# Kernel tuning notes

Measured on AMD Instinct MI355X. Metric: run time of the kernel, lower is better.

The kernel has to match this reference:

```python
import jax, jax.numpy as jnp
import numpy as np

NUM_HEADS = 32
NUM_KV_HEADS = 8
HEAD_DIM = 128
SCALE = 0.08838834764831845  # head_dim ** -0.5
LENS = [1024, 900, 800, 700, 600, 500, 400, 300]  # ragged sequence lengths


def setup_inputs() -> dict:
    key = jax.random.key(0)
    kq, kk, kv = jax.random.split(key, 3)
    cu = np.concatenate([[0], np.cumsum(LENS)]).astype(np.int32)
    T = int(cu[-1])  # 5224 total tokens
    q = jax.random.normal(kq, (T, NUM_HEADS * HEAD_DIM), jnp.float32)
    k = jax.random.normal(kk, (T, NUM_KV_HEADS * HEAD_DIM), jnp.float32)
    v = jax.random.normal(kv, (T, NUM_KV_HEADS * HEAD_DIM), jnp.float32)
    return {"q": q, "k": k, "v": v, "cu_seqlens": jnp.asarray(cu), "max_seqlen": 1024}


def _varlen_indices(cu_seqlens, total_tokens):
    # For each flat token, which sequence it belongs to and its position within it.
    pos = jnp.arange(total_tokens)
    seq_idx = jnp.searchsorted(cu_seqlens[1:], pos, side='right')
    pos_idx = pos - cu_seqlens[seq_idx]
    return seq_idx, pos_idx


def reference(q, k, v, cu_seqlens, max_seqlen):
    T = q.shape[0]
    B = cu_seqlens.shape[0] - 1
    q = q.reshape(T, NUM_HEADS, HEAD_DIM)
    k = k.reshape(T, NUM_KV_HEADS, HEAD_DIM)
    v = v.reshape(T, NUM_KV_HEADS, HEAD_DIM)
    si, pi = _varlen_indices(cu_seqlens, T)

    # varlen -> padded [B, L, H, D] (scatter)
    def pad(x):
        return jnp.zeros((B, max_seqlen) + x.shape[1:], x.dtype).at[si, pi].set(x)

    qp, kp, vp = pad(q), pad(k), pad(v)

    # GQA: repeat_interleave KV heads to match query heads
    rep = NUM_HEADS // NUM_KV_HEADS
    kp = jnp.repeat(kp, rep, axis=2)
    vp = jnp.repeat(vp, rep, axis=2)

    # causal SDPA on padded tensors
    scores = jnp.einsum('bihd,bjhd->bhij', qp, kp) * SCALE  # [B,H,L,L]
    causal = jnp.tril(jnp.ones((max_seqlen, max_seqlen), bool))
    scores = jnp.where(causal, scores, -jnp.inf)
    attn = jax.nn.softmax(scores, axis=-1)
    op = jnp.einsum('bhij,bjhd->bihd', attn, vp)  # [B,L,H,D]

    # padded -> varlen [T, H, D] (gather)
    return op[si, pi]
```

## Files before the change

### kernel.cpp

```cpp
#include <hip/hip_runtime.h>
#include <math.h>

#define NUM_HEADS 32
#define NUM_KV_HEADS 8
#define HEAD_DIM 128
#define QSTRIDE 4096
#define KSTRIDE 1024
#define SCALE 0.08838834764831845f
#define BM 128
#define BN 32
#define PSP 72
#define K1C (SCALE * 1.4426950408889634f)
#define K2C (6.0f * 1.4426950408889634f)
#define KHALF 4096
#define VHALF 4096

typedef __attribute__((ext_vector_type(8))) short short8;
typedef __attribute__((ext_vector_type(16))) float floatx16;
typedef __attribute__((ext_vector_type(4))) float f32x4;

__constant__ unsigned char PERM41[41] = {
  7, 15, 6, 14, 21, 5, 13, 20, 26, 31, 4, 12, 19, 25, 35, 30,
  3, 11, 18, 24, 34, 38, 29, 2, 10, 17, 23, 33, 37, 40, 28,
  1, 9, 16, 22, 32, 36, 39, 27, 0, 8};

__device__ __forceinline__ ushort f2bf(float f) {
  union { float f; unsigned u; } x; x.f = f;
  unsigned r = x.u + 0x7fffu + ((x.u >> 16) & 1u);
  return (ushort)(r >> 16);
}

__device__ __forceinline__ void async16(ushort* lds, const ushort* g) {
  __builtin_amdgcn_global_load_lds(
      (const __attribute__((address_space(1))) unsigned*)g,
      (__attribute__((address_space(3))) unsigned*)lds, 16, 0, 0);
}

__device__ __forceinline__ unsigned cvtpk(float lo, float hi) {
  unsigned r;
  asm("v_cvt_pk_bf16_f32 %0, %1, %2" : "=v"(r) : "v"(lo), "v"(hi));
  return r;
}

__global__ __launch_bounds__(256)
void prep(const float* __restrict__ k, const float* __restrict__ v,
          ushort* __restrict__ kb, ushort* __restrict__ vt,
          int T, int Tpad, int kblk, long nkpad) {
  __shared__ __align__(16) ushort Ls[128][PSP];
  if ((int)blockIdx.x < kblk) {
    long i = ((long)blockIdx.x * 256 + threadIdx.x) * 8;
    if (i >= nkpad) return;
    long lim = (long)T * KSTRIDE;
    ushort w[8] = {0, 0, 0, 0, 0, 0, 0, 0};
    if (i < lim) {
      float4 a = *(const float4*)(k + i);
      float4 b = *(const float4*)(k + i + 4);
      w[0] = f2bf(a.x); w[1] = f2bf(a.y); w[2] = f2bf(a.z); w[3] = f2bf(a.w);
      w[4] = f2bf(b.x); w[5] = f2bf(b.y); w[6] = f2bf(b.z); w[7] = f2bf(b.w);
    }
    *(short8*)(kb + i) = *(short8*)w;
  } else {
    int vb = (int)blockIdx.x - kblk;
    const int kt = (vb >> 3) * 64;
    const int kvh = vb & 7;
    const int j = threadIdx.x >> 2;
    const int dc = (threadIdx.x & 3) * 32;
    const int t = kt + j;
    const float* gv = v + (size_t)t * KSTRIDE + kvh * HEAD_DIM + dc;
    #pragma unroll
    for (int i = 0; i < 32; i += 4) {
      float4 x = (t < T) ? *(const float4*)(gv + i) : make_float4(0.f, 0.f, 0.f, 0.f);
      Ls[dc + i + 0][j] = f2bf(x.x);
      Ls[dc + i + 1][j] = f2bf(x.y);
      Ls[dc + i + 2][j] = f2bf(x.z);
      Ls[dc + i + 3][j] = f2bf(x.w);
    }
    __syncthreads();
    const int d = threadIdx.x >> 1;
    const int k0 = (threadIdx.x & 1) * 32;
    ushort* g = vt + (size_t)(kvh * HEAD_DIM + d) * Tpad + kt + k0;
    #pragma unroll
    for (int i = 0; i < 32; i += 8)
      *(short8*)(g + i) = *(short8*)&Ls[d][k0 + i];
  }
}

__global__ __launch_bounds__(256, 4)
void fa_kernel(const float* __restrict__ q, const ushort* __restrict__ kb,
               const ushort* __restrict__ vt, const int* __restrict__ cu,
               float* __restrict__ out, int T, int Tpad, int B, int nt) {
  const int tid = threadIdx.x;
  const int wave = tid >> 6;
  const int lane = tid & 63;
  const int l32 = lane & 31;
  const int half = lane >> 5;
  const int xr = l32 & 7;
  const int h = ((int)blockIdx.x & 7) * 4 + ((int)blockIdx.x >> 3);
  const int kvh = h >> 2;
  const int tile = (nt == 41) ? (int)PERM41[blockIdx.y] : (nt - 1 - (int)blockIdx.y);
  const int row0 = tile * BM;

  __shared__ __align__(16) ushort KsL[2 * KHALF];
  __shared__ __align__(16) ushort VtL[2 * VHALF];
  __shared__ int rstart[BM], rtok[BM];

  if (tid < BM) {
    int t = row0 + tid;
    int st = 0, tkk = -1;
    if (t < T) {
      int s = 0;
      while (s < B - 1 && cu[s + 1] <= t) s++;
      st = cu[s]; tkk = t;
    }
    rstart[tid] = st; rtok[tid] = tkk;
  }

  size_t koff[2], voff[2];
  int soff[2];
  #pragma unroll
  for (int i = 0; i < 2; i++) {
    int c = wave * 2 + i;
    int r = c * 4 + (lane >> 4);
    int js = lane & 15;
    int j = (js & 8) | ((js ^ (r & 7)) & 7);
    koff[i] = (size_t)r * KSTRIDE + kvh * HEAD_DIM + j * 8;
    int d = c * 16 + (lane >> 2);
    int j2 = (lane & 3) ^ (d & 3);
    voff[i] = (size_t)(kvh * HEAD_DIM + d) * Tpad + j2 * 8;
    soff[i] = c * 512;
  }

  __syncthreads();

  const int kt0 = (rstart[0] / BN) * BN;
  const int tmax = min(row0 + BM - 1, T - 1);
  const int rs_q = rstart[wave * 32 + l32];
  const int tk_q = rtok[wave * 32 + l32];

  #pragma unroll
  for (int i = 0; i < 2; i++) async16(KsL + soff[i], kb + (size_t)kt0 * KSTRIDE + koff[i]);
  #pragma unroll
  for (int i = 0; i < 2; i++) async16(VtL + soff[i], vt + voff[i] + kt0);

  short8 aq[8];
  {
    int myrow = row0 + wave * 32 + l32;
    if (myrow < T) {
      const float* gq = q + (size_t)myrow * QSTRIDE + h * HEAD_DIM + half * 8;
      #pragma unroll
      for (int s = 0; s < 8; s++) {
        f32x4 x = __builtin_nontemporal_load((const f32x4*)(gq + s * 16));
        f32x4 y = __builtin_nontemporal_load((const f32x4*)(gq + s * 16 + 4));
        ushort w[8] = {f2bf(x.x), f2bf(x.y), f2bf(x.z), f2bf(x.w),
                       f2bf(y.x), f2bf(y.y), f2bf(y.z), f2bf(y.w)};
        aq[s] = *(short8*)w;
      }
    } else {
      #pragma unroll
      for (int s = 0; s < 8; s++) aq[s] = (short8){0, 0, 0, 0, 0, 0, 0, 0};
    }
  }

  floatx16 o0 = {0.f,0.f,0.f,0.f,0.f,0.f,0.f,0.f,0.f,0.f,0.f,0.f,0.f,0.f,0.f,0.f};
  floatx16 o1 = o0, o2 = o0, o3 = o0;
  float sm = 0.f;

  __syncthreads();

  int cur = 0;
  for (int kt = kt0; kt <= tmax; kt += BN, cur ^= 1) {
    const ushort* Ks = KsL + cur * KHALF;
    const ushort* Vt = VtL + cur * VHALF;

    int ktn = kt + BN;
    if (ktn <= tmax) {
      ushort* kd = KsL + (cur ^ 1) * KHALF;
      ushort* vd = VtL + (cur ^ 1) * VHALF;
      #pragma unroll
      for (int i = 0; i < 2; i++) async16(kd + soff[i], kb + (size_t)ktn * KSTRIDE + koff[i]);
      #pragma unroll
      for (int i = 0; i < 2; i++) async16(vd + soff[i], vt + voff[i] + ktn);
    }

    floatx16 c0 = {0.f,0.f,0.f,0.f,0.f,0.f,0.f,0.f,0.f,0.f,0.f,0.f,0.f,0.f,0.f,0.f};
    __builtin_amdgcn_s_setprio(1);
    #pragma unroll
    for (int s = 0; s < 8; s++) {
      int jj = 2 * s + half;
      int jsw = (jj & 8) | ((jj ^ xr) & 7);
      const short8 b0 = *(const short8*)&Ks[l32 * 128 + jsw * 8];
      c0 = __builtin_amdgcn_mfma_f32_32x32x16_bf16(b0, aq[s], c0, 0, 0, 0);
    }
    __builtin_amdgcn_s_setprio(0);

    const bool fullt = __all((rs_q <= kt) & (tk_q >= kt + BN - 1));

    #pragma unroll
    for (int g = 0; g < 2; g++) {
      const int r0 = g * 8;
      float p[8];
      if (fullt) {
        #pragma unroll
        for (int jj = 0; jj < 8; jj++)
          p[jj] = __builtin_amdgcn_exp2f(fmaf(c0[r0 + jj], K1C, -K2C));
      } else {
        int kbase = kt + 16 * g + 4 * half;
        #pragma unroll
        for (int jj = 0; jj < 8; jj++) {
          int key = kbase + (jj & 3) + 8 * (jj >> 2);
          bool vld = (key >= rs_q) & (key <= tk_q);
          p[jj] = vld ? __builtin_amdgcn_exp2f(fmaf(c0[r0 + jj], K1C, -K2C)) : 0.f;
        }
      }
      sm += ((p[0] + p[1]) + (p[2] + p[3])) + ((p[4] + p[5]) + (p[6] + p[7]));
      unsigned w0 = cvtpk(p[0], p[1]);
      unsigned w1 = cvtpk(p[2], p[3]);
      unsigned w2 = cvtpk(p[4], p[5]);
      unsigned w3 = cvtpk(p[6], p[7]);
      asm("v_permlane32_swap_b32 %0, %1" : "+v"(w0), "+v"(w2));
      asm("v_permlane32_swap_b32 %0, %1" : "+v"(w1), "+v"(w3));
      union { unsigned u[4]; short8 s8; } ap;
      ap.u[0] = w0; ap.u[1] = w1; ap.u[2] = w2; ap.u[3] = w3;
      int j2r = (2 * g + half) ^ (l32 & 3);
      const ushort* Vb = Vt + l32 * 32 + j2r * 8;
      o0 = __builtin_amdgcn_mfma_f32_32x32x16_bf16(ap.s8, *(const short8*)(Vb), o0, 0, 0, 0);
      o1 = __builtin_amdgcn_mfma_f32_32x32x16_bf16(ap.s8, *(const short8*)(Vb + 1024), o1, 0, 0, 0);
      o2 = __builtin_amdgcn_mfma_f32_32x32x16_bf16(ap.s8, *(const short8*)(Vb + 2048), o2, 0, 0, 0);
      o3 = __builtin_amdgcn_mfma_f32_32x32x16_bf16(ap.s8, *(const short8*)(Vb + 3072), o3, 0, 0, 0);
    }

    __syncthreads();
  }

  float smT = sm + __shfl_xor(sm, 32, 64);
  #pragma unroll
  for (int r = 0; r < 16; r++) {
    int qr = (r & 3) + 8 * (r >> 2) + 4 * half;
    float dn = __shfl(smT, qr, 64);
    int tkr = rtok[wave * 32 + qr];
    if (tkr >= 0) {
      float inv = 1.f / dn;
      float* go = out + (size_t)tkr * QSTRIDE + h * HEAD_DIM + l32;
      __builtin_nontemporal_store(o0[r] * inv, go);
      __builtin_nontemporal_store(o1[r] * inv, go + 32);
      __builtin_nontemporal_store(o2[r] * inv, go + 64);
      __builtin_nontemporal_store(o3[r] * inv, go + 96);
    }
  }
}

extern "C" void kernel_launch(void* const* d_in, const int* in_sizes, int n_in,
                              void* d_out, int out_size, void* d_ws, size_t ws_size,
                              hipStream_t stream) {
  const float* q = (const float*)d_in[0];
  const float* k = (const float*)d_in[1];
  const float* v = (const float*)d_in[2];
  const int* cu = (const int*)d_in[3];
  float* out = (float*)d_out;
  int T = in_sizes[0] / QSTRIDE;
  int B = in_sizes[3] - 1;
  int Tpad = ((T + 63) / 64) * 64;

  ushort* kb = (ushort*)d_ws;
  ushort* vt = kb + (size_t)Tpad * 1024;

  long nkpad = (long)Tpad * KSTRIDE;
  int kblk = (int)((nkpad / 8 + 255) / 256);
  int vblk = (Tpad / 64) * NUM_KV_HEADS;
  hipLaunchKernelGGL(prep, dim3(kblk + vblk), dim3(256), 0, stream,
                     k, v, kb, vt, T, Tpad, kblk, nkpad);
  int nt = (T + BM - 1) / BM;
  hipLaunchKernelGGL(fa_kernel, dim3(NUM_HEADS, nt), dim3(256), 0, stream,
                     q, kb, vt, cu, out, T, Tpad, B, nt);
}
```

Before: 300.5 us.

## Pre-swizzle K/V into MFMA fragment layout and load directly to registers

The prep kernel now writes K and V in bf16, pre-arranged into per-lane MFMA fragment order. The attention kernel can then load fragments straight from global memory into registers, with no LDS staging, async copies or per-iteration block barriers. K fragments for the next tile are prefetched into registers, and QK uses two accumulator chains that are summed afterwards. Occupancy drops to 2 blocks per CU in exchange for the larger register use, and each wave now does its own global loads, relying on L2 hits instead of shared LDS reuse across waves.

```diff
diff --git a/kernel.cpp b/kernel.cpp
--- a/kernel.cpp
+++ b/kernel.cpp
@@ -8,12 +8,9 @@
 #define KSTRIDE 1024
 #define SCALE 0.08838834764831845f
 #define BM 128
-#define BN 32
 #define PSP 72
 #define K1C (SCALE * 1.4426950408889634f)
 #define K2C (6.0f * 1.4426950408889634f)
-#define KHALF 4096
-#define VHALF 4096
 
 typedef __attribute__((ext_vector_type(8))) short short8;
 typedef __attribute__((ext_vector_type(16))) float floatx16;
@@ -30,12 +27,6 @@
   return (ushort)(r >> 16);
 }
 
-__device__ __forceinline__ void async16(ushort* lds, const ushort* g) {
-  __builtin_amdgcn_global_load_lds(
-      (const __attribute__((address_space(1))) unsigned*)g,
-      (__attribute__((address_space(3))) unsigned*)lds, 16, 0, 0);
-}
-
 __device__ __forceinline__ unsigned cvtpk(float lo, float hi) {
   unsigned r;
   asm("v_cvt_pk_bf16_f32 %0, %1, %2" : "=v"(r) : "v"(lo), "v"(hi));
@@ -44,192 +35,170 @@
 
 __global__ __launch_bounds__(256)
 void prep(const float* __restrict__ k, const float* __restrict__ v,
-          ushort* __restrict__ kb, ushort* __restrict__ vt,
-          int T, int Tpad, int kblk, long nkpad) {
-  __shared__ __align__(16) ushort Ls[128][PSP];
-  if ((int)blockIdx.x < kblk) {
-    long i = ((long)blockIdx.x * 256 + threadIdx.x) * 8;
-    if (i >= nkpad) return;
-    long lim = (long)T * KSTRIDE;
-    ushort w[8] = {0, 0, 0, 0, 0, 0, 0, 0};
-    if (i < lim) {
-      float4 a = *(const float4*)(k + i);
-      float4 b = *(const float4*)(k + i + 4);
-      w[0] = f2bf(a.x); w[1] = f2bf(a.y); w[2] = f2bf(a.z); w[3] = f2bf(a.w);
-      w[4] = f2bf(b.x); w[5] = f2bf(b.y); w[6] = f2bf(b.z); w[7] = f2bf(b.w);
-    }
-    *(short8*)(kb + i) = *(short8*)w;
-  } else {
-    int vb = (int)blockIdx.x - kblk;
-    const int kt = (vb >> 3) * 64;
-    const int kvh = vb & 7;
-    const int j = threadIdx.x >> 2;
+          ushort* __restrict__ kfr, ushort* __restrict__ vfr,
+          int T, int NB32, int NB16) {
+  const int kt = (int)blockIdx.x * 64;
+  const int kvh = (int)blockIdx.y;
+  __shared__ __align__(16) ushort Kt[64][136];
+  __shared__ __align__(16) ushort Vs[128][PSP];
+  {
+    const int key = threadIdx.x >> 2;
     const int dc = (threadIdx.x & 3) * 32;
-    const int t = kt + j;
-    const float* gv = v + (size_t)t * KSTRIDE + kvh * HEAD_DIM + dc;
+    const bool inb = (kt + key) < T;
+    const float* gk = k + (size_t)(kt + key) * KSTRIDE + kvh * HEAD_DIM + dc;
+    const float* gv = v + (size_t)(kt + key) * KSTRIDE + kvh * HEAD_DIM + dc;
+    #pragma unroll
+    for (int i = 0; i < 32; i += 8) {
+      float4 a = inb ? *(const float4*)(gk + i) : make_float4(0.f, 0.f, 0.f, 0.f);
+      float4 b = inb ? *(const float4*)(gk + i + 4) : make_float4(0.f, 0.f, 0.f, 0.f);
+      ushort w[8] = {f2bf(a.x), f2bf(a.y), f2bf(a.z), f2bf(a.w),
+                     f2bf(b.x), f2bf(b.y), f2bf(b.z), f2bf(b.w)};
+      *(short8*)&Kt[key][dc + i] = *(short8*)w;
+    }
     #pragma unroll
     for (int i = 0; i < 32; i += 4) {
-      float4 x = (t < T) ? *(const float4*)(gv + i) : make_float4(0.f, 0.f, 0.f, 0.f);
-      Ls[dc + i + 0][j] = f2bf(x.x);
-      Ls[dc + i + 1][j] = f2bf(x.y);
-      Ls[dc + i + 2][j] = f2bf(x.z);
-      Ls[dc + i + 3][j] = f2bf(x.w);
-    }
-    __syncthreads();
-    const int d = threadIdx.x >> 1;
-    const int k0 = (threadIdx.x & 1) * 32;
-    ushort* g = vt + (size_t)(kvh * HEAD_DIM + d) * Tpad + kt + k0;
-    #pragma unroll
-    for (int i = 0; i < 32; i += 8)
-      *(short8*)(g + i) = *(short8*)&Ls[d][k0 + i];
-  }
-}
-
-__global__ __launch_bounds__(256, 4)
-void fa_kernel(const float* __restrict__ q, const ushort* __restrict__ kb,
-               const ushort* __restrict__ vt, const int* __restrict__ cu,
-               float* __restrict__ out, int T, int Tpad, int B, int nt) {
+      float4 x = inb ? *(const float4*)(gv + i) : make_float4(0.f, 0.f, 0.f, 0.f);
+      Vs[dc + i + 0][key] = f2bf(x.x);
+      Vs[dc + i + 1][key] = f2bf(x.y);
+      Vs[dc + i + 2][key] = f2bf(x.z);
+      Vs[dc + i + 3][key] = f2bf(x.w);
+    }
+  }
+  __syncthreads();
+  const int l = threadIdx.x & 63;
+  const int wv = threadIdx.x >> 6;
+  const int l32 = l & 31;
+  const int hb = l >> 5;
+  #pragma unroll
+  for (int q0 = 0; q0 < 4; q0++) {
+    int c = q0 * 4 + wv;
+    int kb2 = c >> 3, s = c & 7;
+    short8 d = *(const short8*)&Kt[kb2 * 32 + l32][s * 16 + hb * 8];
+    *(short8*)(kfr + ((size_t)(kvh * NB32 + (kt >> 5) + kb2) * 8 + s) * 512 + l * 8) = d;
+  }
+  #pragma unroll
+  for (int q0 = 0; q0 < 4; q0++) {
+    int c = q0 * 4 + wv;
+    int kb = c >> 2, i = c & 3;
+    short8 d = *(const short8*)&Vs[i * 32 + l32][kb * 16 + hb * 8];
+    *(short8*)(vfr + ((size_t)(kvh * NB16 + (kt >> 4) + kb) * 4 + i) * 512 + l * 8) = d;
+  }
+}
+
+__global__ __launch_bounds__(256, 2)
+void fa_kernel(const float* __restrict__ q, const ushort* __restrict__ kfr,
+               const ushort* __restrict__ vfr, const int* __restrict__ cu,
+               float* __restrict__ out, int T, int NB32, int NB16, int B, int nt) {
   const int tid = threadIdx.x;
   const int wave = tid >> 6;
   const int lane = tid & 63;
   const int l32 = lane & 31;
   const int half = lane >> 5;
-  const int xr = l32 & 7;
   const int h = ((int)blockIdx.x & 7) * 4 + ((int)blockIdx.x >> 3);
   const int kvh = h >> 2;
   const int tile = (nt == 41) ? (int)PERM41[blockIdx.y] : (nt - 1 - (int)blockIdx.y);
   const int row0 = tile * BM;
-
-  __shared__ __align__(16) ushort KsL[2 * KHALF];
-  __shared__ __align__(16) ushort VtL[2 * VHALF];
-  __shared__ int rstart[BM], rtok[BM];
-
-  if (tid < BM) {
-    int t = row0 + tid;
-    int st = 0, tkk = -1;
-    if (t < T) {
-      int s = 0;
-      while (s < B - 1 && cu[s + 1] <= t) s++;
-      st = cu[s]; tkk = t;
-    }
-    rstart[tid] = st; rtok[tid] = tkk;
-  }
-
-  size_t koff[2], voff[2];
-  int soff[2];
-  #pragma unroll
-  for (int i = 0; i < 2; i++) {
-    int c = wave * 2 + i;
-    int r = c * 4 + (lane >> 4);
-    int js = lane & 15;
-    int j = (js & 8) | ((js ^ (r & 7)) & 7);
-    koff[i] = (size_t)r * KSTRIDE + kvh * HEAD_DIM + j * 8;
-    int d = c * 16 + (lane >> 2);
-    int j2 = (lane & 3) ^ (d & 3);
-    voff[i] = (size_t)(kvh * HEAD_DIM + d) * Tpad + j2 * 8;
-    soff[i] = c * 512;
-  }
-
-  __syncthreads();
-
-  const int kt0 = (rstart[0] / BN) * BN;
+  const int myrow = row0 + wave * 32 + l32;
+
+  int rs_q = 0, tk_q = -1;
+  if (myrow < T) {
+    int s = 0;
+    while (s < B - 1 && cu[s + 1] <= myrow) s++;
+    rs_q = cu[s]; tk_q = myrow;
+  }
+  int s0 = 0;
+  while (s0 < B - 1 && cu[s0 + 1] <= row0) s0++;
+  const int kt0 = (cu[s0] / 32) * 32;
   const int tmax = min(row0 + BM - 1, T - 1);
-  const int rs_q = rstart[wave * 32 + l32];
-  const int tk_q = rtok[wave * 32 + l32];
-
-  #pragma unroll
-  for (int i = 0; i < 2; i++) async16(KsL + soff[i], kb + (size_t)kt0 * KSTRIDE + koff[i]);
-  #pragma unroll
-  for (int i = 0; i < 2; i++) async16(VtL + soff[i], vt + voff[i] + kt0);
 
   short8 aq[8];
+  if (myrow < T) {
+    const float* gq = q + (size_t)myrow * QSTRIDE + h * HEAD_DIM + half * 8;
+    #pragma unroll
+    for (int s = 0; s < 8; s++) {
+      f32x4 x = __builtin_nontemporal_load((const f32x4*)(gq + s * 16));
+      f32x4 y = __builtin_nontemporal_load((const f32x4*)(gq + s * 16 + 4));
+      ushort w[8] = {f2bf(x.x), f2bf(x.y), f2bf(x.z), f2bf(x.w),
+                     f2bf(y.x), f2bf(y.y), f2bf(y.z), f2bf(y.w)};
+      aq[s] = *(short8*)w;
+    }
+  } else {
+    #pragma unroll
+    for (int s = 0; s < 8; s++) aq[s] = (short8){0, 0, 0, 0, 0, 0, 0, 0};
+  }
+
+  const ushort* kbase = kfr + (size_t)kvh * NB32 * 4096 + lane * 8;
+  const ushort* vbase = vfr + (size_t)kvh * NB16 * 2048 + lane * 8;
+
+  short8 kf[8];
   {
-    int myrow = row0 + wave * 32 + l32;
-    if (myrow < T) {
-      const float* gq = q + (size_t)myrow * QSTRIDE + h * HEAD_DIM + half * 8;
-      #pragma unroll
-      for (int s = 0; s < 8; s++) {
-        f32x4 x = __builtin_nontemporal_load((const f32x4*)(gq + s * 16));
-        f32x4 y = __builtin_nontemporal_load((const f32x4*)(gq + s * 16 + 4));
-        ushort w[8] = {f2bf(x.x), f2bf(x.y), f2bf(x.z), f2bf(x.w),
-                       f2bf(y.x), f2bf(y.y), f2bf(y.z), f2bf(y.w)};
-        aq[s] = *(short8*)w;
-      }
-    } else {
-      #pragma unroll
-      for (int s = 0; s < 8; s++) aq[s] = (short8){0, 0, 0, 0, 0, 0, 0, 0};
-    }
+    const ushort* kp = kbase + (size_t)(kt0 >> 5) * 4096;
+    #pragma unroll
+    for (int s = 0; s < 8; s++) kf[s] = *(const short8*)(kp + s * 512);
   }
 
   floatx16 o0 = {0.f,0.f,0.f,0.f,0.f,0.f,0.f,0.f,0.f,0.f,0.f,0.f,0.f,0.f,0.f,0.f};
   floatx16 o1 = o0, o2 = o0, o3 = o0;
   float sm = 0.f;
 
-  __syncthreads();
-
-  int cur = 0;
-  for (int kt = kt0; kt <= tmax; kt += BN, cur ^= 1) {
-    const ushort* Ks = KsL + cur * KHALF;
-    const ushort* Vt = VtL + cur * VHALF;
-
-    int ktn = kt + BN;
-    if (ktn <= tmax) {
-      ushort* kd = KsL + (cur ^ 1) * KHALF;
-      ushort* vd = VtL + (cur ^ 1) * VHALF;
-      #pragma unroll
-      for (int i = 0; i < 2; i++) async16(kd + soff[i], kb + (size_t)ktn * KSTRIDE + koff[i]);
-      #pragma unroll
-      for (int i = 0; i < 2; i++) async16(vd + soff[i], vt + voff[i] + ktn);
-    }
-
-    floatx16 c0 = {0.f,0.f,0.f,0.f,0.f,0.f,0.f,0.f,0.f,0.f,0.f,0.f,0.f,0.f,0.f,0.f};
+  for (int kt = kt0; kt <= tmax; kt += 32) {
+    short8 vf[8];
+    {
+      const ushort* vp = vbase + (size_t)(kt >> 4) * 2048;
+      #pragma unroll
+      for (int c = 0; c < 8; c++) vf[c] = *(const short8*)(vp + c * 512);
+    }
+
+    floatx16 ca = {0.f,0.f,0.f,0.f,0.f,0.f,0.f,0.f,0.f,0.f,0.f,0.f,0.f,0.f,0.f,0.f};
+    floatx16 cb = ca;
     __builtin_amdgcn_s_setprio(1);
     #pragma unroll
-    for (int s = 0; s < 8; s++) {
-      int jj = 2 * s + half;
-      int jsw = (jj & 8) | ((jj ^ xr) & 7);
-      const short8 b0 = *(const short8*)&Ks[l32 * 128 + jsw * 8];
-      c0 = __builtin_amdgcn_mfma_f32_32x32x16_bf16(b0, aq[s], c0, 0, 0, 0);
+    for (int s = 0; s < 8; s += 2) {
+      ca = __builtin_amdgcn_mfma_f32_32x32x16_bf16(kf[s], aq[s], ca, 0, 0, 0);
+      cb = __builtin_amdgcn_mfma_f32_32x32x16_bf16(kf[s + 1], aq[s + 1], cb, 0, 0, 0);
     }
     __builtin_amdgcn_s_setprio(0);
 
-    const bool fullt = __all((rs_q <= kt) & (tk_q >= kt + BN - 1));
+    {
+      int ktn = kt + 32;
+      const ushort* kp = kbase + (size_t)(((ktn <= tmax) ? ktn : kt0) >> 5) * 4096;
+      #pragma unroll
+      for (int s = 0; s < 8; s++) kf[s] = *(const short8*)(kp + s * 512);
+    }
+
+    const bool fullt = __all((rs_q <= kt) & (tk_q >= kt + 31));
+    if (fullt) {
+      #pragma unroll
+      for (int r = 0; r < 16; r++) {
+        ca[r] = __builtin_amdgcn_exp2f(fmaf(ca[r] + cb[r], K1C, -K2C));
+        sm += ca[r];
+      }
+    } else {
+      #pragma unroll
+      for (int r = 0; r < 16; r++) {
+        int key = kt + (r & 3) + 8 * (r >> 2) + 4 * half;
+        bool vld = (key >= rs_q) & (key <= tk_q);
+        ca[r] = vld ? __builtin_amdgcn_exp2f(fmaf(ca[r] + cb[r], K1C, -K2C)) : 0.f;
+        sm += ca[r];
+      }
+    }
 
     #pragma unroll
     for (int g = 0; g < 2; g++) {
       const int r0 = g * 8;
-      float p[8];
-      if (fullt) {
-        #pragma unroll
-        for (int jj = 0; jj < 8; jj++)
-          p[jj] = __builtin_amdgcn_exp2f(fmaf(c0[r0 + jj], K1C, -K2C));
-      } else {
-        int kbase = kt + 16 * g + 4 * half;
-        #pragma unroll
-        for (int jj = 0; jj < 8; jj++) {
-          int key = kbase + (jj & 3) + 8 * (jj >> 2);
-          bool vld = (key >= rs_q) & (key <= tk_q);
-          p[jj] = vld ? __builtin_amdgcn_exp2f(fmaf(c0[r0 + jj], K1C, -K2C)) : 0.f;
-        }
-      }
-      sm += ((p[0] + p[1]) + (p[2] + p[3])) + ((p[4] + p[5]) + (p[6] + p[7]));
-      unsigned w0 = cvtpk(p[0], p[1]);
-      unsigned w1 = cvtpk(p[2], p[3]);
-      unsigned w2 = cvtpk(p[4], p[5]);
-      unsigned w3 = cvtpk(p[6], p[7]);
+      unsigned w0 = cvtpk(ca[r0 + 0], ca[r0 + 1]);
+      unsigned w1 = cvtpk(ca[r0 + 2], ca[r0 + 3]);
+      unsigned w2 = cvtpk(ca[r0 + 4], ca[r0 + 5]);
+      unsigned w3 = cvtpk(ca[r0 + 6], ca[r0 + 7]);
       asm("v_permlane32_swap_b32 %0, %1" : "+v"(w0), "+v"(w2));
       asm("v_permlane32_swap_b32 %0, %1" : "+v"(w1), "+v"(w3));
       union { unsigned u[4]; short8 s8; } ap;
       ap.u[0] = w0; ap.u[1] = w1; ap.u[2] = w2; ap.u[3] = w3;
-      int j2r = (2 * g + half) ^ (l32 & 3);
-      const ushort* Vb = Vt + l32 * 32 + j2r * 8;
-      o0 = __builtin_amdgcn_mfma_f32_32x32x16_bf16(ap.s8, *(const short8*)(Vb), o0, 0, 0, 0);
-      o1 = __builtin_amdgcn_mfma_f32_32x32x16_bf16(ap.s8, *(const short8*)(Vb + 1024), o1, 0, 0, 0);
-      o2 = __builtin_amdgcn_mfma_f32_32x32x16_bf16(ap.s8, *(const short8*)(Vb + 2048), o2, 0, 0, 0);
-      o3 = __builtin_amdgcn_mfma_f32_32x32x16_bf16(ap.s8, *(const short8*)(Vb + 3072), o3, 0, 0, 0);
-    }
-
-    __syncthreads();
+      o0 = __builtin_amdgcn_mfma_f32_32x32x16_bf16(ap.s8, vf[g * 4 + 0], o0, 0, 0, 0);
+      o1 = __builtin_amdgcn_mfma_f32_32x32x16_bf16(ap.s8, vf[g * 4 + 1], o1, 0, 0, 0);
+      o2 = __builtin_amdgcn_mfma_f32_32x32x16_bf16(ap.s8, vf[g * 4 + 2], o2, 0, 0, 0);
+      o3 = __builtin_amdgcn_mfma_f32_32x32x16_bf16(ap.s8, vf[g * 4 + 3], o3, 0, 0, 0);
+    }
   }
 
   float smT = sm + __shfl_xor(sm, 32, 64);
@@ -237,7 +206,7 @@
   for (int r = 0; r < 16; r++) {
     int qr = (r & 3) + 8 * (r >> 2) + 4 * half;
     float dn = __shfl(smT, qr, 64);
-    int tkr = rtok[wave * 32 + qr];
+    int tkr = __shfl(tk_q, qr, 64);
     if (tkr >= 0) {
       float inv = 1.f / dn;
       float* go = out + (size_t)tkr * QSTRIDE + h * HEAD_DIM + l32;
@@ -260,16 +229,14 @@
   int T = in_sizes[0] / QSTRIDE;
   int B = in_sizes[3] - 1;
   int Tpad = ((T + 63) / 64) * 64;
-
-  ushort* kb = (ushort*)d_ws;
-  ushort* vt = kb + (size_t)Tpad * 1024;
-
-  long nkpad = (long)Tpad * KSTRIDE;
-  int kblk = (int)((nkpad / 8 + 255) / 256);
-  int vblk = (Tpad / 64) * NUM_KV_HEADS;
-  hipLaunchKernelGGL(prep, dim3(kblk + vblk), dim3(256), 0, stream,
-                     k, v, kb, vt, T, Tpad, kblk, nkpad);
+  int NB32 = Tpad / 32, NB16 = Tpad / 16;
+
+  ushort* kfr = (ushort*)d_ws;
+  ushort* vfr = kfr + (size_t)Tpad * 1024;
+
+  hipLaunchKernelGGL(prep, dim3(Tpad / 64, NUM_KV_HEADS), dim3(256), 0, stream,
+                     k, v, kfr, vfr, T, NB32, NB16);
   int nt = (T + BM - 1) / BM;
   hipLaunchKernelGGL(fa_kernel, dim3(NUM_HEADS, nt), dim3(256), 0, stream,
-                     q, kb, vt, cu, out, T, Tpad, B, nt);
-}
+                     q, kfr, vfr, cu, out, T, NB32, NB16, B, nt);
+}
```

New measurement: 251.8 us. -16.2%, faster.
